# Optimization experiments

Hardware: AMD Instinct MI355X
Metric: run time of the kernel (lower is better)

Reference implementation:

```python
import jax, jax.numpy as jnp
import numpy as np

N = 50000      # nodes
E = 800000     # edges
D = 128        # hidden_channels
H = 4          # heads
DH = D // H    # per-head dim


def setup_inputs() -> dict:
    key = jax.random.key(0)
    ks = jax.random.split(key, 10)
    s = 1.0 / np.sqrt(D)
    x = jax.random.normal(ks[0], (N, D), dtype=jnp.float32)
    edge_index = jax.random.randint(ks[1], (2, E), 0, N, dtype=jnp.int64)
    Wq = jax.random.normal(ks[2], (D, D), dtype=jnp.float32) * s
    bq = jnp.zeros((D,), dtype=jnp.float32)
    Wk = jax.random.normal(ks[3], (D, D), dtype=jnp.float32) * s
    bk = jnp.zeros((D,), dtype=jnp.float32)
    Wv = jax.random.normal(ks[4], (D, D), dtype=jnp.float32) * s
    bv = jnp.zeros((D,), dtype=jnp.float32)
    Wskip = jax.random.normal(ks[5], (D, D), dtype=jnp.float32) * s
    bskip = jnp.zeros((D,), dtype=jnp.float32)
    return {"x": x, "edge_index": edge_index, "Wq": Wq, "bq": bq,
            "Wk": Wk, "bk": bk, "Wv": Wv, "bv": bv,
            "Wskip": Wskip, "bskip": bskip}


def reference(x, edge_index, Wq, bq, Wk, bk, Wv, bv, Wskip, bskip):
    # MixerBlock.forward: x + TransformerConv(x, edge_index)
    src = edge_index[0]  # source (message sender) j
    dst = edge_index[1]  # destination (aggregating) i

    q = (x @ Wq.T + bq).reshape(N, H, DH)
    k = (x @ Wk.T + bk).reshape(N, H, DH)
    v = (x @ Wv.T + bv).reshape(N, H, DH)

    q_e = q[dst]          # [E, H, DH] gather per edge
    k_e = k[src]
    v_e = v[src]

    # per-edge, per-head attention logits
    alpha = jnp.sum(q_e * k_e, axis=-1) / jnp.sqrt(jnp.float32(DH))  # [E, H]

    # segment softmax over edges grouped by destination node (PyG softmax)
    m = jax.ops.segment_max(alpha, dst, num_segments=N)   # [N, H]
    a = jnp.exp(alpha - m[dst])                           # [E, H]
    denom = jax.ops.segment_sum(a, dst, num_segments=N)   # [N, H]
    a = a / (denom[dst] + 1e-16)

    # scatter-aggregate weighted values
    out = jax.ops.segment_sum(a[..., None] * v_e, dst, num_segments=N)  # [N, H, DH]
    out = out.reshape(N, D)

    # root/skip connection inside TransformerConv (root_weight=True)
    out = out + x @ Wskip.T + bskip

    # residual in MixerBlock.forward
    return x + out
```

## Files before the change

kernel.cpp:

```cpp
#include <hip/hip_runtime.h>
#include <math.h>

#define D 128
#define MAXBIN 1600

typedef __attribute__((ext_vector_type(8))) short short8;
typedef __attribute__((ext_vector_type(4))) float f32x4;
typedef __attribute__((ext_vector_type(2))) float f32x2;

__device__ __forceinline__ ushort f2bf(float f) {
    uint u = __float_as_uint(f);
    u += 0x7FFFu + ((u >> 16) & 1u);
    return (ushort)(u >> 16);
}
__device__ __forceinline__ float bf2f(ushort h) { return __uint_as_float(((uint)h) << 16); }
__device__ __forceinline__ float lo2f(uint u) { return __uint_as_float(u << 16); }
__device__ __forceinline__ float hi2f(uint u) { return __uint_as_float(u & 0xFFFF0000u); }

__global__ void convertW_kernel(
    const float* __restrict__ Wq, const float* __restrict__ Wk,
    const float* __restrict__ Wv, const float* __restrict__ Ws,
    ushort* __restrict__ wb)
{
    int i = blockIdx.x * 256 + threadIdx.x;
    if (i < 16384) {
        int m = i >> 12;
        const float* W = (m == 0) ? Wq : (m == 1) ? Wk : (m == 2) ? Wv : Ws;
        float4 f = ((const float4*)W)[i & 4095];
        ushort4 h;
        h.x = f2bf(f.x); h.y = f2bf(f.y); h.z = f2bf(f.z); h.w = f2bf(f.w);
        ((ushort4*)wb)[i] = h;
    }
}

__global__ __launch_bounds__(512) void fused_mfma_hist(
    const float* __restrict__ x, const ushort* __restrict__ wb,
    const float* __restrict__ bq, const float* __restrict__ bk,
    const float* __restrict__ bv, const float* __restrict__ bsk,
    ushort* __restrict__ qb, uchar* __restrict__ kvrow,
    float* __restrict__ out, int N,
    const int* __restrict__ dst, int* __restrict__ ghist,
    int E, int RB, int NBIN)
{
    __shared__ __align__(16) uchar  xs[64 * 256];
    __shared__ __align__(16) ushort stg[8][16][64];
    __shared__ int hbin[MAXBIN];

    const int bid = blockIdx.x;
    const int ri  = bid / 3;
    if ((bid % 3 == 1) && (ri < RB)) {
        for (int j = threadIdx.x; j < NBIN; j += 512) hbin[j] = 0;
        __syncthreads();
        const int base = ri * 2048;
        #pragma unroll
        for (int k = 0; k < 4; ++k) {
            const int e = base + k * 512 + (int)threadIdx.x;
            if (e < E) atomicAdd(&hbin[dst[e] >> 5], 1);
        }
        __syncthreads();
        int* gh = ghist + (size_t)ri * NBIN;
        for (int j = threadIdx.x; j < NBIN; j += 512) gh[j] = hbin[j];
        return;
    }
    const int mb = bid - min((bid + 1) / 3, RB);

    const int t = threadIdx.x;
    const int w = t >> 6, l = t & 63;
    const int mat = w >> 1;
    const int col0 = (w & 1) * 64;
    const int r0 = mb * 64;
    const int lr = l & 15, lg = l >> 4;

    #pragma unroll
    for (int rr = 0; rr < 4; ++rr) {
        const int idx = rr * 512 + t;
        const int row = idx >> 5;
        const int c4  = idx & 31;
        float4 f = make_float4(0.f, 0.f, 0.f, 0.f);
        const int gr = r0 + row;
        if (gr < N) f = *(const float4*)(x + (size_t)gr * D + c4 * 4);
        uint2 h;
        h.x = (uint)f2bf(f.x) | ((uint)f2bf(f.y) << 16);
        h.y = (uint)f2bf(f.z) | ((uint)f2bf(f.w) << 16);
        const int baddr = (row * 256 + c4 * 8) ^ ((row & 7) << 4);
        *(uint2*)(xs + baddr) = h;
    }
    __syncthreads();

    const ushort* W = wb + (size_t)mat * (D * D);
    const float* bias = (mat == 0) ? bq : (mat == 1) ? bk : (mat == 2) ? bv : bsk;

    float bi[4];
    #pragma unroll
    for (int ct = 0; ct < 4; ++ct) bi[ct] = bias[col0 + ct * 16 + lr];

    f32x4 acc[4][4];
    #pragma unroll
    for (int rt = 0; rt < 4; ++rt)
        #pragma unroll
        for (int ct = 0; ct < 4; ++ct)
            acc[rt][ct] = (f32x4){0.f, 0.f, 0.f, 0.f};

    #pragma unroll
    for (int ks = 0; ks < 4; ++ks) {
        const int kbyte = ks * 64 + lg * 16;
        short8 b[4];
        #pragma unroll
        for (int ct = 0; ct < 4; ++ct)
            b[ct] = *(const short8*)(W + (size_t)(col0 + ct * 16 + lr) * D + ks * 32 + lg * 8);
        short8 a[4];
        #pragma unroll
        for (int rt = 0; rt < 4; ++rt) {
            const int rowL = rt * 16 + lr;
            a[rt] = *(const short8*)(xs + ((rowL * 256 + kbyte) ^ ((rowL & 7) << 4)));
        }
        #pragma unroll
        for (int rt = 0; rt < 4; ++rt)
            #pragma unroll
            for (int ct = 0; ct < 4; ++ct)
                acc[rt][ct] = __builtin_amdgcn_mfma_f32_16x16x32_bf16(
                    a[rt], b[ct], acc[rt][ct], 0, 0, 0);
    }

    for (int rt = 0; rt < 4; ++rt) {
        #pragma unroll
        for (int ct = 0; ct < 4; ++ct) {
            const int colL = ct * 16 + lr;
            const int cch = colL >> 3, cin = colL & 7;
            #pragma unroll
            for (int r = 0; r < 4; ++r) {
                const int rowL = lg * 4 + r;
                stg[w][rowL][((cch ^ (rowL & 7)) << 3) + cin] =
                    f2bf(acc[rt][ct][r] + bi[ct]);
            }
        }
        #pragma unroll
        for (int rr = 0; rr < 2; ++rr) {
            const int rowL = rr * 8 + (l >> 3);
            const int c = l & 7;
            const int p = c ^ (rowL & 7);
            uint4 hv = *(const uint4*)&stg[w][rowL][p << 3];
            const int row_g = r0 + rt * 16 + rowL;
            if (row_g < N) {
                if (mat == 0) {
                    *(uint4*)(qb + (size_t)row_g * D + col0 + c * 8) = hv;
                } else if (mat == 1) {
                    const uint* hu = (const uint*)&hv;
                    uint w0 = 0, w1 = 0;
                    w0 = __builtin_amdgcn_cvt_pk_fp8_f32(lo2f(hu[0]), hi2f(hu[0]), w0, false);
                    w0 = __builtin_amdgcn_cvt_pk_fp8_f32(lo2f(hu[1]), hi2f(hu[1]), w0, true);
                    w1 = __builtin_amdgcn_cvt_pk_fp8_f32(lo2f(hu[2]), hi2f(hu[2]), w1, false);
                    w1 = __builtin_amdgcn_cvt_pk_fp8_f32(lo2f(hu[3]), hi2f(hu[3]), w1, true);
                    uint2 pk; pk.x = w0; pk.y = w1;
                    *(uint2*)(kvrow + (size_t)row_g * 384 + col0 + c * 8) = pk;
                } else if (mat == 2) {
                    *(uint4*)(kvrow + (size_t)row_g * 384 + 128 + 2 * col0 + 16 * c) = hv;
                } else {
                    const ushort* hs = (const ushort*)&hv;
                    const float4* xr = (const float4*)(x + (size_t)row_g * D + col0 + c * 8);
                    float4 x0 = xr[0], x1 = xr[1];
                    float4 o0, o1;
                    o0.x = x0.x + bf2f(hs[0]); o0.y = x0.y + bf2f(hs[1]);
                    o0.z = x0.z + bf2f(hs[2]); o0.w = x0.w + bf2f(hs[3]);
                    o1.x = x1.x + bf2f(hs[4]); o1.y = x1.y + bf2f(hs[5]);
                    o1.z = x1.z + bf2f(hs[6]); o1.w = x1.w + bf2f(hs[7]);
                    float4* orow = (float4*)(out + (size_t)row_g * D + col0 + c * 8);
                    orow[0] = o0; orow[1] = o1;
                }
            }
        }
    }
}

__global__ __launch_bounds__(256) void binscan_kernel(
    int* __restrict__ ghist, int* __restrict__ T, int NBIN, int EBK)
{
    const int bin  = blockIdx.x * 4 + ((int)threadIdx.x >> 6);
    const int lane = threadIdx.x & 63;
    if (bin >= NBIN) return;
    int running = 0;
    for (int s = 0; s < EBK; s += 64) {
        const int k = s + lane;
        int v = (k < EBK) ? ghist[(size_t)k * NBIN + bin] : 0;
        const int orig = v;
        #pragma unroll
        for (int off = 1; off < 64; off <<= 1) {
            int u = __shfl_up(v, off);
            if (lane >= off) v += u;
        }
        if (k < EBK) ghist[(size_t)k * NBIN + bin] = running + v - orig;
        running += __shfl(v, 63);
    }
    if (lane == 0) T[bin] = running;
}

__global__ void tscan_kernel(const int* __restrict__ T, int* __restrict__ Tofs, int NBIN)
{
    const int lane = threadIdx.x;
    int base = 0;
    for (int s = 0; s < NBIN; s += 64) {
        const int idx = s + lane;
        int v = (idx < NBIN) ? T[idx] : 0;
        const int orig = v;
        #pragma unroll
        for (int off = 1; off < 64; off <<= 1) {
            int u = __shfl_up(v, off);
            if (lane >= off) v += u;
        }
        if (idx < NBIN) Tofs[idx] = base + v - orig;
        base += __shfl(v, 63);
    }
    if (lane == 0) Tofs[NBIN] = base;
}

__global__ __launch_bounds__(512) void bucket_scatter_kernel(
    const int* __restrict__ src, const int* __restrict__ dst,
    const int* __restrict__ ghist, const int* __restrict__ Tofs,
    int* __restrict__ ssrc, ushort* __restrict__ sdst, int E, int NBIN)
{
    __shared__ int cur[MAXBIN];
    const int ri = blockIdx.x;
    const int* gh = ghist + (size_t)ri * NBIN;
    for (int j = threadIdx.x; j < NBIN; j += 512) cur[j] = Tofs[j] + gh[j];
    __syncthreads();
    const int base = ri * 2048;
    #pragma unroll
    for (int k = 0; k < 4; ++k) {
        const int e = base + k * 512 + (int)threadIdx.x;
        if (e < E) {
            const int d = dst[e];
            const int p = atomicAdd(&cur[d >> 5], 1);
            ssrc[p] = src[e] * 384;
            sdst[p] = (ushort)d;
        }
    }
}

__global__ __launch_bounds__(512) void finalize_kernel(
    const int* __restrict__ ssrc, const ushort* __restrict__ sdst,
    const int* __restrict__ Tofs, int* __restrict__ edge_src,
    int* __restrict__ counts, int* __restrict__ offsets, int NBIN, int N)
{
    __shared__ int cnt[32], pref[32], cur[32];
    const int b = blockIdx.x;
    const int t = threadIdx.x;
    const int start = Tofs[b];
    const int end   = Tofs[b + 1];

    if (t < 32) cnt[t] = 0;
    __syncthreads();
    for (int e = start + t; e < end; e += 512)
        atomicAdd(&cnt[sdst[e] & 31], 1);
    __syncthreads();
    if (t < 64) {
        int v = (t < 32) ? cnt[t] : 0;
        #pragma unroll
        for (int off = 1; off < 32; off <<= 1) {
            int u = __shfl_up(v, off);
            if ((t & 63) >= off) v += u;
        }
        if (t < 32) { pref[t] = v - cnt[t]; cur[t] = v - cnt[t]; }
    }
    __syncthreads();
    for (int e = start + t; e < end; e += 512) {
        const int ld = sdst[e] & 31;
        const int p = atomicAdd(&cur[ld], 1);
        edge_src[start + p] = ssrc[e];
    }
    if (t < 32) {
        const int node = b * 32 + t;
        if (node < N) {
            counts[node]  = cnt[t];
            offsets[node] = start + pref[t];
        }
    }
}

__global__ __launch_bounds__(256) void attn_kernel(
    const ushort* __restrict__ qb, const uchar* __restrict__ kvrow,
    const int* __restrict__ counts, const int* __restrict__ offsets,
    const int* __restrict__ edge_src, float* __restrict__ out, int N)
{
    const int lane = threadIdx.x & 63;
    const int slot = lane >> 4;
    const int ld   = lane & 15;
    const int wv   = threadIdx.x >> 6;
    const int i    = blockIdx.x * 4 + wv;
    if (i >= N) return;

    const float scale = 0.17677669529663687f;
    const uint4 qa = *(const uint4*)(qb + (size_t)i * D + 8 * ld);
    float qf[8];
    qf[0] = lo2f(qa.x) * scale; qf[1] = hi2f(qa.x) * scale;
    qf[2] = lo2f(qa.y) * scale; qf[3] = hi2f(qa.y) * scale;
    qf[4] = lo2f(qa.z) * scale; qf[5] = hi2f(qa.z) * scale;
    qf[6] = lo2f(qa.w) * scale; qf[7] = hi2f(qa.w) * scale;

    const int beg = offsets[i];
    const int cnt = counts[i];

    float l = 0.f;
    float av[8] = {0.f, 0.f, 0.f, 0.f, 0.f, 0.f, 0.f, 0.f};

    if (cnt > 0) {
        const int last = beg + cnt - 1;
        const uchar* kb = kvrow + 8 * ld;
        const uchar* vb = kvrow + 128 + 16 * ld;

        uint2 kk; uint4 vv;
        {
            const int off = edge_src[min(beg + slot, last)];
            kk = *(const uint2*)(kb + off);
            vv = *(const uint4*)(vb + off);
        }

        for (int e = 0; e < cnt; e += 4) {
            uint2 nk; uint4 nv;
            {
                const int off = edge_src[min(beg + e + 4 + slot, last)];
                nk = *(const uint2*)(kb + off);
                nv = *(const uint4*)(vb + off);
            }

            const f32x2 k01 = __builtin_amdgcn_cvt_pk_f32_fp8(kk.x, false);
            const f32x2 k23 = __builtin_amdgcn_cvt_pk_f32_fp8(kk.x, true);
            const f32x2 k45 = __builtin_amdgcn_cvt_pk_f32_fp8(kk.y, false);
            const f32x2 k67 = __builtin_amdgcn_cvt_pk_f32_fp8(kk.y, true);
            float dp;
            dp  = qf[0] * k01.x + qf[1] * k01.y;
            dp += qf[2] * k23.x + qf[3] * k23.y;
            dp += qf[4] * k45.x + qf[5] * k45.y;
            dp += qf[6] * k67.x + qf[7] * k67.y;
            dp += __shfl_xor(dp, 1);
            dp += __shfl_xor(dp, 2);

            const float p = (e + slot < cnt) ? __expf(dp) : 0.f;

            l += p;
            av[0] = fmaf(p, lo2f(vv.x), av[0]);
            av[1] = fmaf(p, hi2f(vv.x), av[1]);
            av[2] = fmaf(p, lo2f(vv.y), av[2]);
            av[3] = fmaf(p, hi2f(vv.y), av[3]);
            av[4] = fmaf(p, lo2f(vv.z), av[4]);
            av[5] = fmaf(p, hi2f(vv.z), av[5]);
            av[6] = fmaf(p, lo2f(vv.w), av[6]);
            av[7] = fmaf(p, hi2f(vv.w), av[7]);
            kk = nk; vv = nv;
        }
    }

    #pragma unroll
    for (int dist = 16; dist <= 32; dist <<= 1) {
        l += __shfl_xor(l, dist);
        #pragma unroll
        for (int d = 0; d < 8; ++d) av[d] += __shfl_xor(av[d], dist);
    }

    if (slot == 0) {
        const float inv = 1.0f / (l + 1e-16f);
        float4* orow = (float4*)(out + (size_t)i * D + 8 * ld);
        float4 o0 = orow[0], o1 = orow[1];
        o0.x += av[0] * inv; o0.y += av[1] * inv;
        o0.z += av[2] * inv; o0.w += av[3] * inv;
        o1.x += av[4] * inv; o1.y += av[5] * inv;
        o1.z += av[6] * inv; o1.w += av[7] * inv;
        orow[0] = o0; orow[1] = o1;
    }
}

extern "C" void kernel_launch(void* const* d_in, const int* in_sizes, int n_in,
                              void* d_out, int out_size, void* d_ws, size_t ws_size,
                              hipStream_t stream)
{
    const float* x   = (const float*)d_in[0];
    const int*   ei  = (const int*)d_in[1];
    const float* Wq  = (const float*)d_in[2];
    const float* bq  = (const float*)d_in[3];
    const float* Wk  = (const float*)d_in[4];
    const float* bk  = (const float*)d_in[5];
    const float* Wv  = (const float*)d_in[6];
    const float* bv  = (const float*)d_in[7];
    const float* Wsk = (const float*)d_in[8];
    const float* bsk = (const float*)d_in[9];
    float* out = (float*)d_out;

    const int N = in_sizes[0] / D;
    const int E = in_sizes[1] / 2;
    const int NBIN = (N + 31) / 32;
    const int EBK  = (E + 2047) / 2048;

    char* ws = (char*)d_ws;
    size_t o = 0;
    ushort* wb      = (ushort*)(ws + o); o += (size_t)4 * D * D * sizeof(ushort);
    ushort* qb      = (ushort*)(ws + o); o += (size_t)N * D * sizeof(ushort);
    uchar*  kvrow   = (uchar*)(ws + o);  o += (size_t)N * 384;
    o = (o + 255) & ~(size_t)255;
    int*    ghist   = (int*)(ws + o);    o += (size_t)EBK * NBIN * sizeof(int);
    int*    T       = (int*)(ws + o);    o += (size_t)NBIN * sizeof(int);
    int*    Tofs    = (int*)(ws + o);    o += (size_t)(NBIN + 1) * sizeof(int);
    int*    ssrc    = (int*)(ws + o);    o += (size_t)E * sizeof(int);
    ushort* sdst    = (ushort*)(ws + o); o += (size_t)E * sizeof(ushort);
    o = (o + 255) & ~(size_t)255;
    int*    counts  = (int*)(ws + o);    o += (size_t)N * sizeof(int);
    int*    offsets = (int*)(ws + o);    o += (size_t)N * sizeof(int);
    int*    edge_src= (int*)(ws + o);    o += (size_t)E * sizeof(int);

    convertW_kernel<<<64, 256, 0, stream>>>(Wq, Wk, Wv, Wsk, wb);

    const int MB = (N + 63) / 64;
    fused_mfma_hist<<<MB + EBK, 512, 0, stream>>>(
        x, wb, bq, bk, bv, bsk, qb, kvrow, out, N,
        ei + E, ghist, E, EBK, NBIN);

    binscan_kernel<<<(NBIN + 3) / 4, 256, 0, stream>>>(ghist, T, NBIN, EBK);
    tscan_kernel<<<1, 64, 0, stream>>>(T, Tofs, NBIN);

    bucket_scatter_kernel<<<EBK, 512, 0, stream>>>(
        ei, ei + E, ghist, Tofs, ssrc, sdst, E, NBIN);

    finalize_kernel<<<NBIN, 512, 0, stream>>>(
        ssrc, sdst, Tofs, edge_src, counts, offsets, NBIN, N);

    attn_kernel<<<(N + 3) / 4, 256, 0, stream>>>(qb, kvrow, counts, offsets, edge_src, out, N);
}
```

Measured before the change: 146.2 us.

## Enlarge histogram chunks, reuse shared memory, and simplify bin scan

Each histogram/scatter block now covers 8192 edges instead of 2048, so there are four times fewer chunks and a smaller per-chunk histogram matrix to scan and read back. Histogram blocks are placed first in the fused launch instead of interleaved, and they reuse the xs shared buffer instead of a separate array, which cuts static LDS use for the GEMM blocks. The bin scan becomes a plain sequential per-thread loop over the fewer chunks. In exchange, the bucket scatter launches fewer, longer blocks, which may lower parallelism and increase atomic contention per block.

```diff
diff --git a/kernel.cpp b/kernel.cpp
--- a/kernel.cpp
+++ b/kernel.cpp
@@ -40,29 +40,28 @@
     ushort* __restrict__ qb, uchar* __restrict__ kvrow,
     float* __restrict__ out, int N,
     const int* __restrict__ dst, int* __restrict__ ghist,
-    int E, int RB, int NBIN)
+    int E, int EBK, int NBIN)
 {
     __shared__ __align__(16) uchar  xs[64 * 256];
     __shared__ __align__(16) ushort stg[8][16][64];
-    __shared__ int hbin[MAXBIN];
 
     const int bid = blockIdx.x;
-    const int ri  = bid / 3;
-    if ((bid % 3 == 1) && (ri < RB)) {
+    if (bid < EBK) {
+        int* hbin = (int*)xs;
         for (int j = threadIdx.x; j < NBIN; j += 512) hbin[j] = 0;
         __syncthreads();
-        const int base = ri * 2048;
-        #pragma unroll
-        for (int k = 0; k < 4; ++k) {
+        const int base = bid * 8192;
+        #pragma unroll
+        for (int k = 0; k < 16; ++k) {
             const int e = base + k * 512 + (int)threadIdx.x;
             if (e < E) atomicAdd(&hbin[dst[e] >> 5], 1);
         }
         __syncthreads();
-        int* gh = ghist + (size_t)ri * NBIN;
+        int* gh = ghist + (size_t)bid * NBIN;
         for (int j = threadIdx.x; j < NBIN; j += 512) gh[j] = hbin[j];
         return;
     }
-    const int mb = bid - min((bid + 1) / 3, RB);
+    const int mb = bid - EBK;
 
     const int t = threadIdx.x;
     const int w = t >> 6, l = t & 63;
@@ -175,23 +174,16 @@
 __global__ __launch_bounds__(256) void binscan_kernel(
     int* __restrict__ ghist, int* __restrict__ T, int NBIN, int EBK)
 {
-    const int bin  = blockIdx.x * 4 + ((int)threadIdx.x >> 6);
-    const int lane = threadIdx.x & 63;
-    if (bin >= NBIN) return;
-    int running = 0;
-    for (int s = 0; s < EBK; s += 64) {
-        const int k = s + lane;
-        int v = (k < EBK) ? ghist[(size_t)k * NBIN + bin] : 0;
-        const int orig = v;
-        #pragma unroll
-        for (int off = 1; off < 64; off <<= 1) {
-            int u = __shfl_up(v, off);
-            if (lane >= off) v += u;
-        }
-        if (k < EBK) ghist[(size_t)k * NBIN + bin] = running + v - orig;
-        running += __shfl(v, 63);
-    }
-    if (lane == 0) T[bin] = running;
+    const int b = blockIdx.x * 256 + threadIdx.x;
+    if (b >= NBIN) return;
+    int run = 0;
+    for (int k = 0; k < EBK; ++k) {
+        int* p = ghist + (size_t)k * NBIN + b;
+        const int v = *p;
+        *p = run;
+        run += v;
+    }
+    T[b] = run;
 }
 
 __global__ void tscan_kernel(const int* __restrict__ T, int* __restrict__ Tofs, int NBIN)
@@ -223,9 +215,9 @@
     const int* gh = ghist + (size_t)ri * NBIN;
     for (int j = threadIdx.x; j < NBIN; j += 512) cur[j] = Tofs[j] + gh[j];
     __syncthreads();
-    const int base = ri * 2048;
-    #pragma unroll
-    for (int k = 0; k < 4; ++k) {
+    const int base = ri * 8192;
+    #pragma unroll
+    for (int k = 0; k < 16; ++k) {
         const int e = base + k * 512 + (int)threadIdx.x;
         if (e < E) {
             const int d = dst[e];
@@ -387,7 +379,7 @@
     const int N = in_sizes[0] / D;
     const int E = in_sizes[1] / 2;
     const int NBIN = (N + 31) / 32;
-    const int EBK  = (E + 2047) / 2048;
+    const int EBK  = (E + 8191) / 8192;
 
     char* ws = (char*)d_ws;
     size_t o = 0;
@@ -408,11 +400,11 @@
     convertW_kernel<<<64, 256, 0, stream>>>(Wq, Wk, Wv, Wsk, wb);
 
     const int MB = (N + 63) / 64;
-    fused_mfma_hist<<<MB + EBK, 512, 0, stream>>>(
+    fused_mfma_hist<<<EBK + MB, 512, 0, stream>>>(
         x, wb, bq, bk, bv, bsk, qb, kvrow, out, N,
         ei + E, ghist, E, EBK, NBIN);
 
-    binscan_kernel<<<(NBIN + 3) / 4, 256, 0, stream>>>(ghist, T, NBIN, EBK);
+    binscan_kernel<<<(NBIN + 255) / 256, 256, 0, stream>>>(ghist, T, NBIN, EBK);
     tscan_kernel<<<1, 64, 0, stream>>>(T, Tofs, NBIN);
 
     bucket_scatter_kernel<<<EBK, 512, 0, stream>>>(
```

New measurement: 158.0 us. +8.1%, slower.
